# Optimization experiments

Measured on AMD Instinct MI355X. Metric: run time of the kernel, lower is better.

The kernel has to match this reference:

```python
import jax, jax.numpy as jnp
import numpy as np

N, E = 50000, 800000
D, H, EDIM, DFF = 128, 8, 16, 512
C = D // H  # per-head channels
NEG_SLOPE_GAT = 0.2
NEG_SLOPE = 0.01
EPS_LN = 1e-6


def layer_norm(x, g, b):
    mu = x.mean(-1, keepdims=True)
    sd = x.std(-1, keepdims=True, ddof=1)  # torch std default (unbiased)
    return g * (x - mu) / (sd + EPS_LN) + b


def gat_conv(x, ei, ew, W, a_src, a_dst, We, a_e, bias):
    # PyG GATConv with edge_dim, concat=True, eval mode (no dropout)
    n = x.shape[0]
    xh = (x @ W).reshape(n, H, C)            # [N,H,C]
    s_src = (xh * a_src).sum(-1)             # [N,H]
    s_dst = (xh * a_dst).sum(-1)             # [N,H]
    eh = (ew @ We).reshape(-1, H, C)         # [E,H,C]
    s_e = (eh * a_e).sum(-1)                 # [E,H]
    src, dst = ei[0], ei[1]
    alpha = jax.nn.leaky_relu(s_src[src] + s_dst[dst] + s_e, NEG_SLOPE_GAT)  # [E,H]
    # segment softmax over destination nodes
    m = jax.ops.segment_max(alpha, dst, num_segments=n)
    alpha = jnp.exp(alpha - m[dst])
    z = jax.ops.segment_sum(alpha, dst, num_segments=n)
    alpha = alpha / (z[dst] + 1e-16)
    msg = xh[src] * alpha[..., None]         # [E,H,C]
    out = jax.ops.segment_sum(msg, dst, num_segments=n)  # [N,H,C]
    return out.reshape(n, H * C) + bias


def setup_inputs() -> dict:
    key = jax.random.key(0)
    ks = jax.random.split(key, 32)
    p = lambda k, sh: (jax.random.normal(k, sh, dtype=jnp.float32) * 0.02)
    inp = {
        "nf": jax.random.normal(ks[0], (N, D), dtype=jnp.float32),
        "ei": jax.random.randint(ks[1], (2, E), 0, N, dtype=jnp.int32),
        "ew": jax.random.normal(ks[2], (E, EDIM), dtype=jnp.float32),
        # GATConv 1
        "W1": p(ks[3], (D, H * C)), "as1": p(ks[4], (H, C)), "ad1": p(ks[5], (H, C)),
        "We1": p(ks[6], (EDIM, H * C)), "ae1": p(ks[7], (H, C)), "b1": jnp.zeros((H * C,), jnp.float32),
        "g1": jnp.ones((D,), jnp.float32), "be1": jnp.zeros((D,), jnp.float32),
        # GATConv 2
        "W2": p(ks[8], (D, H * C)), "as2": p(ks[9], (H, C)), "ad2": p(ks[10], (H, C)),
        "We2": p(ks[11], (EDIM, H * C)), "ae2": p(ks[12], (H, C)), "b2": jnp.zeros((H * C,), jnp.float32),
        "g2": jnp.ones((D,), jnp.float32), "be2": jnp.zeros((D,), jnp.float32),
        # FFN + norm3
        "Wf1": p(ks[13], (D, DFF)), "bf1": jnp.zeros((DFF,), jnp.float32),
        "Wf2": p(ks[14], (DFF, D)), "bf2": jnp.zeros((D,), jnp.float32),
        "g3": jnp.ones((D,), jnp.float32), "be3": jnp.zeros((D,), jnp.float32),
    }
    return inp


def reference(nf, ei, ew, W1, as1, ad1, We1, ae1, b1, g1, be1,
              W2, as2, ad2, We2, ae2, b2, g2, be2,
              Wf1, bf1, Wf2, bf2, g3, be3):
    # gnn_mode == 'res', eval mode (dropout = identity)
    h = gat_conv(nf, ei, ew, W1, as1, ad1, We1, ae1, b1)
    nf = nf + jax.nn.leaky_relu(layer_norm(h, g1, be1), NEG_SLOPE)
    h = gat_conv(nf, ei, ew, W2, as2, ad2, We2, ae2, b2)
    nf = nf + jax.nn.leaky_relu(layer_norm(h, g2, be2), NEG_SLOPE)
    ff = jax.nn.relu(nf @ Wf1 + bf1) @ Wf2 + bf2
    nf = nf + jax.nn.leaky_relu(layer_norm(ff, g3, be3), NEG_SLOPE)
    return nf
```

## Files before the change

kernel.cpp:

```cpp
#include <hip/hip_runtime.h>
#include <hip/hip_bf16.h>

#define NN 50000
#define NE 800000
#define DD 128
#define HH 8
#define CC 16
#define DFF 512
#define ED 16
#define SCAN_NB ((NN + 255) / 256)
#define BKT 256
#define NBKT ((NN + BKT - 1) / BKT)
#define EPB 4096

typedef __attribute__((ext_vector_type(8))) short bf16x8;
typedef __attribute__((ext_vector_type(4))) float f32x4;

union U8 { bf16x8 v; unsigned short s[8]; };

__device__ inline unsigned short f2bf(float f) {
    union { float f; unsigned u; } v; v.f = f;
    return (unsigned short)((v.u + 0x7fffu + ((v.u >> 16) & 1u)) >> 16);
}
__device__ inline float bf2f(unsigned s) {
    union { unsigned u; float f; } v; v.u = s << 16;
    return v.f;
}

__global__ void zero_int_k(int* __restrict__ a, int n) {
    int i = blockIdx.x * 256 + threadIdx.x;
    if (i < n) a[i] = 0;
}

__global__ void cvtpack_k(const float* __restrict__ W, unsigned short* __restrict__ Wpk,
                          int K, int N) {
    int idx = blockIdx.x * 256 + threadIdx.x;
    if (idx >= K * N) return;
    int e = idx & 7;
    int l = (idx >> 3) & 63;
    int r = idx >> 9;
    int n16 = N >> 4;
    int jc = r % n16;
    int kt = r / n16;
    int k = kt * 32 + (l >> 4) * 8 + e;
    int n = jc * 16 + (l & 15);
    Wpk[idx] = f2bf(W[(size_t)k * N + n]);
}

__global__ void count_k(const int* __restrict__ dst, int* __restrict__ cnt) {
    int e = blockIdx.x * 256 + threadIdx.x;
    if (e < NE) atomicAdd(&cnt[dst[e]], 1);
}

__global__ void blksum_k(const int* __restrict__ cnt, int* __restrict__ partials) {
    int i = blockIdx.x * 256 + threadIdx.x;
    int v = (i < NN) ? cnt[i] : 0;
#pragma unroll
    for (int m = 1; m < 64; m <<= 1) v += __shfl_xor(v, m, 64);
    __shared__ int ws[4];
    if ((threadIdx.x & 63) == 0) ws[threadIdx.x >> 6] = v;
    __syncthreads();
    if (threadIdx.x == 0) partials[blockIdx.x] = ws[0] + ws[1] + ws[2] + ws[3];
}

__global__ void scanpart_k(int* __restrict__ partials) {
    __shared__ int buf[256];
    int t = threadIdx.x;
    int v = (t < SCAN_NB) ? partials[t] : 0;
    buf[t] = v;
    __syncthreads();
    for (int off = 1; off < 256; off <<= 1) {
        int u = (t >= off) ? buf[t - off] : 0;
        __syncthreads();
        buf[t] += u;
        __syncthreads();
    }
    if (t < SCAN_NB) partials[t] = buf[t] - v;
}

__global__ void scanapply_k(const int* __restrict__ cnt, const int* __restrict__ partials,
                            int* __restrict__ row_start, int* __restrict__ cursor) {
    __shared__ int buf[256];
    int t = threadIdx.x;
    int i = blockIdx.x * 256 + t;
    int v = (i < NN) ? cnt[i] : 0;
    buf[t] = v;
    __syncthreads();
    for (int off = 1; off < 256; off <<= 1) {
        int u = (t >= off) ? buf[t - off] : 0;
        __syncthreads();
        buf[t] += u;
        __syncthreads();
    }
    int excl = buf[t] - v + partials[blockIdx.x];
    if (i < NN) {
        row_start[i] = excl;
        cursor[i] = excl;
        if (i == NN - 1) row_start[NN] = excl + v;
    }
}

__global__ void bucketbase_k(const int* __restrict__ row_start, int* __restrict__ bucket_cursor) {
    int b = blockIdx.x * 256 + threadIdx.x;
    if (b < NBKT) bucket_cursor[b] = row_start[b * BKT];
}

__global__ __launch_bounds__(256) void bin_k(const int* __restrict__ ei,
                                             int* __restrict__ bucket_cursor,
                                             int2* __restrict__ binned) {
    __shared__ int hist[NBKT];
    __shared__ int base[NBKT];
    int t = threadIdx.x;
    int e0 = blockIdx.x * EPB;
    int eend = e0 + EPB; if (eend > NE) eend = NE;
    if (t < NBKT) hist[t] = 0;
    __syncthreads();
    for (int e = e0 + t; e < eend; e += 256) {
        int d = ei[NE + e];
        atomicAdd(&hist[d >> 8], 1);
    }
    __syncthreads();
    if (t < NBKT) {
        int c = hist[t];
        base[t] = c ? atomicAdd(&bucket_cursor[t], c) : 0;
        hist[t] = 0;
    }
    __syncthreads();
    for (int e = e0 + t; e < eend; e += 256) {
        int s = ei[e];
        int d = ei[NE + e];
        int b = d >> 8;
        int loc = atomicAdd(&hist[b], 1);
        binned[base[b] + loc] = make_int2(s | ((d & 255) << 16), e);
    }
}

__global__ __launch_bounds__(256) void csr_scatter_k(const int2* __restrict__ binned,
                                                     const int* __restrict__ row_start,
                                                     int* __restrict__ cursor,
                                                     int* __restrict__ e_src,
                                                     int* __restrict__ e_eid) {
    int b = blockIdx.x;
    int beg = row_start[b * BKT];
    int endNode = (b + 1) * BKT; if (endNode > NN) endNode = NN;
    int end = row_start[endNode];
    for (int p = beg + threadIdx.x; p < end; p += 256) {
        int2 r = binned[p];
        int d = b * BKT + (r.x >> 16);
        int pos = atomicAdd(&cursor[d], 1);
        e_src[pos] = r.x & 0xffff;
        e_eid[pos] = r.y;
    }
}

__global__ void se2_k(const float* __restrict__ ew, const int* __restrict__ e_eid,
                      const float* __restrict__ We1, const float* __restrict__ ae1,
                      const float* __restrict__ We2, const float* __restrict__ ae2,
                      unsigned short* __restrict__ s_e1, unsigned short* __restrict__ s_e2) {
    __shared__ float A1[ED * HH], A2[ED * HH];
    int t = threadIdx.x;
    if (t < 128) {
        int k = t >> 3, h = t & 7;
        float s = 0.f;
#pragma unroll
        for (int c = 0; c < CC; c++) s += We1[k * DD + h * CC + c] * ae1[h * CC + c];
        A1[t] = s;
    } else {
        int u = t - 128;
        int k = u >> 3, h = u & 7;
        float s = 0.f;
#pragma unroll
        for (int c = 0; c < CC; c++) s += We2[k * DD + h * CC + c] * ae2[h * CC + c];
        A2[u] = s;
    }
    __syncthreads();
    int p = blockIdx.x * 256 + t;
    if (p >= NE) return;
    int eid = e_eid[p];
    const float* ep = &ew[(size_t)eid * ED];
    float4 v0 = *(const float4*)(ep);
    float4 v1 = *(const float4*)(ep + 4);
    float4 v2 = *(const float4*)(ep + 8);
    float4 v3 = *(const float4*)(ep + 12);
    float ev[16] = {v0.x, v0.y, v0.z, v0.w, v1.x, v1.y, v1.z, v1.w,
                    v2.x, v2.y, v2.z, v2.w, v3.x, v3.y, v3.z, v3.w};
    float o1[8] = {0, 0, 0, 0, 0, 0, 0, 0};
    float o2[8] = {0, 0, 0, 0, 0, 0, 0, 0};
#pragma unroll
    for (int k = 0; k < 16; k++) {
        float v = ev[k];
#pragma unroll
        for (int h = 0; h < 8; h++) {
            o1[h] += v * A1[k * 8 + h];
            o2[h] += v * A2[k * 8 + h];
        }
    }
    U8 w1, w2;
#pragma unroll
    for (int h = 0; h < 8; h++) { w1.s[h] = f2bf(o1[h]); w2.s[h] = f2bf(o2[h]); }
    *(bf16x8*)&s_e1[(size_t)p * 8] = w1.v;
    *(bf16x8*)&s_e2[(size_t)p * 8] = w2.v;
}

__global__ __launch_bounds__(256) void gemm_mfma_k(const float* __restrict__ X,
                                                   const unsigned short* __restrict__ Wpk,
                                                   unsigned short* __restrict__ Ybf) {
    __shared__ char Xl[128 * 256];
    int t = threadIdx.x;
    int nb0 = blockIdx.x * 128;
    for (int c = t; c < 2048; c += 256) {
        int row = c >> 4, cb = c & 15;
        int n = nb0 + row;
        U8 u;
        if (n < NN) {
            const float* xp = &X[(size_t)n * DD + cb * 8];
            float4 a = *(const float4*)xp;
            float4 b = *(const float4*)(xp + 4);
            u.s[0] = f2bf(a.x); u.s[1] = f2bf(a.y); u.s[2] = f2bf(a.z); u.s[3] = f2bf(a.w);
            u.s[4] = f2bf(b.x); u.s[5] = f2bf(b.y); u.s[6] = f2bf(b.z); u.s[7] = f2bf(b.w);
        } else {
#pragma unroll
            for (int q = 0; q < 8; q++) u.s[q] = 0;
        }
        int byte = (row * 256 + cb * 16) ^ ((row & 7) << 4);
        *(bf16x8*)&Xl[byte] = u.v;
    }
    __syncthreads();
    int w = t >> 6, l = t & 63;
    int lrow = l & 15, lq = l >> 4;
    int r0 = (w & 1) * 64, c0 = (w >> 1) * 64;
    f32x4 acc[4][4];
#pragma unroll
    for (int i = 0; i < 4; i++)
#pragma unroll
        for (int j = 0; j < 4; j++) acc[i][j] = (f32x4){0.f, 0.f, 0.f, 0.f};
#pragma unroll
    for (int ks = 0; ks < 4; ks++) {
        int k0 = ks * 32;
        bf16x8 af[4], bq[4];
#pragma unroll
        for (int i = 0; i < 4; i++) {
            int rr = r0 + i * 16 + lrow;
            int byte = (rr * 256 + k0 * 2 + lq * 16) ^ ((rr & 7) << 4);
            af[i] = *(const bf16x8*)&Xl[byte];
        }
#pragma unroll
        for (int j = 0; j < 4; j++) {
            int j16 = (c0 >> 4) + j;
            bq[j] = *(const bf16x8*)&Wpk[(((size_t)ks * 8 + j16) * 64 + l) * 8];
        }
#pragma unroll
        for (int i = 0; i < 4; i++)
#pragma unroll
            for (int j = 0; j < 4; j++)
                acc[i][j] = __builtin_amdgcn_mfma_f32_16x16x32_bf16(af[i], bq[j], acc[i][j], 0, 0, 0);
    }
#pragma unroll
    for (int i = 0; i < 4; i++) {
#pragma unroll
        for (int j = 0; j < 4; j++) {
#pragma unroll
            for (int q = 0; q < 4; q++) {
                int n = nb0 + r0 + i * 16 + lq * 4 + q;
                if (n < NN) Ybf[(size_t)n * DD + c0 + j * 16 + lrow] = f2bf(acc[i][j][q]);
            }
        }
    }
}

__global__ void ssd_k(const unsigned short* __restrict__ xh_bf, const float* __restrict__ a_src,
                      const float* __restrict__ a_dst, unsigned short* __restrict__ s_srcb,
                      float* __restrict__ s_dst) {
    __shared__ float as[128], ad[128];
    if (threadIdx.x < 128) {
        as[threadIdx.x] = a_src[threadIdx.x];
        ad[threadIdx.x] = a_dst[threadIdx.x];
    }
    __syncthreads();
    int idx = blockIdx.x * 256 + threadIdx.x;
    if (idx >= NN * HH) return;
    int n = idx >> 3, h = idx & 7;
    const unsigned short* x = &xh_bf[(size_t)n * DD + h * CC];
    U8 u0, u1;
    u0.v = *(const bf16x8*)(x);
    u1.v = *(const bf16x8*)(x + 8);
    float s1 = 0.f, s2 = 0.f;
#pragma unroll
    for (int c = 0; c < 8; c++) {
        float v = bf2f(u0.s[c]);
        s1 += v * as[h * CC + c];
        s2 += v * ad[h * CC + c];
    }
#pragma unroll
    for (int c = 0; c < 8; c++) {
        float v = bf2f(u1.s[c]);
        s1 += v * as[h * CC + 8 + c];
        s2 += v * ad[h * CC + 8 + c];
    }
    s_srcb[idx] = f2bf(s1);
    s_dst[idx] = s2;
}

__global__ __launch_bounds__(256) void agg_ln_k(const int* __restrict__ row_start,
                                                const int* __restrict__ e_src,
                                                const unsigned short* __restrict__ s_srcb,
                                                const float* __restrict__ s_dst,
                                                const unsigned short* __restrict__ s_eb,
                                                const unsigned short* __restrict__ xh_bf,
                                                const float* __restrict__ bias,
                                                const float* __restrict__ g,
                                                const float* __restrict__ be,
                                                const float* __restrict__ res,
                                                float* __restrict__ outNf) {
    int wid = (blockIdx.x * 256 + threadIdx.x) >> 6;
    if (wid >= NN) return;
    int lane = threadIdx.x & 63;
    int h = lane >> 3;
    int k = lane & 7;
    unsigned h2 = (unsigned)h << 1;
    unsigned loff = (unsigned)lane << 2;
    const char* xb = (const char*)xh_bf;
    const char* sb = (const char*)s_srcb;
    const char* eb = (const char*)s_eb;
    float sdst = s_dst[wid * 8 + h];
    int beg = row_start[wid], end = row_start[wid + 1];
    float acc0 = 0.f, acc1 = 0.f, zpart = 0.f, ztail = 0.f;
    int p = beg;
    int bcast = h << 3;
    for (; p + 8 <= end; p += 8) {
        unsigned q = (unsigned)e_src[p + k];
        float vs = bf2f(*(const unsigned short*)(sb + (q << 4) + h2));
        float ve = bf2f(*(const unsigned short*)(eb + (((unsigned)(p + k)) << 4) + h2));
        float a = vs + sdst + ve;
        a = fmaxf(a, 0.2f * a);
        float esc = __expf(a);
        zpart += esc;
#pragma unroll
        for (int kk = 0; kk < 8; kk++) {
            float sck = __shfl(esc, bcast + kk, 64);
            unsigned qk = (unsigned)__shfl((int)q, kk, 64);
            unsigned u = *(const unsigned*)(xb + (qk << 8) + loff);
            acc0 = fmaf(sck, bf2f(u & 0xffffu), acc0);
            acc1 = fmaf(sck, bf2f(u >> 16), acc1);
        }
    }
    for (; p < end; p++) {
        unsigned q0 = (unsigned)e_src[p];
        float a0 = bf2f(*(const unsigned short*)(sb + (q0 << 4) + h2)) + sdst
                 + bf2f(*(const unsigned short*)(eb + ((unsigned)p << 4) + h2));
        unsigned u0 = *(const unsigned*)(xb + (q0 << 8) + loff);
        a0 = fmaxf(a0, 0.2f * a0);
        float e0 = __expf(a0);
        ztail += e0;
        acc0 = fmaf(e0, bf2f(u0 & 0xffffu), acc0);
        acc1 = fmaf(e0, bf2f(u0 >> 16), acc1);
    }
    float z = zpart;
    z += __shfl_xor(z, 1, 64);
    z += __shfl_xor(z, 2, 64);
    z += __shfl_xor(z, 4, 64);
    z += ztail;
    float inv = 1.f / (z + 1e-16f);
    float2 b = *(const float2*)&bias[lane * 2];
    float x0 = acc0 * inv + b.x;
    float x1 = acc1 * inv + b.y;
    float s = x0 + x1;
    float q = x0 * x0 + x1 * x1;
#pragma unroll
    for (int m = 1; m < 64; m <<= 1) {
        s += __shfl_xor(s, m, 64);
        q += __shfl_xor(q, m, 64);
    }
    float mu = s * (1.f / 128.f);
    float var = (q - 128.f * mu * mu) * (1.f / 127.f);
    float sd = sqrtf(fmaxf(var, 0.f));
    float invs = 1.f / (sd + 1e-6f);
    float2 gg = *(const float2*)&g[lane * 2];
    float2 bb = *(const float2*)&be[lane * 2];
    float y0 = gg.x * (x0 - mu) * invs + bb.x;
    float y1 = gg.y * (x1 - mu) * invs + bb.y;
    y0 = (y0 > 0.f) ? y0 : 0.01f * y0;
    y1 = (y1 > 0.f) ? y1 : 0.01f * y1;
    float2 r = *(const float2*)&res[(size_t)wid * DD + lane * 2];
    *(float2*)&outNf[(size_t)wid * DD + lane * 2] = make_float2(r.x + y0, r.y + y1);
}

__global__ __launch_bounds__(256) void ffn_ln_k(const float* __restrict__ X,
                                                const unsigned short* __restrict__ Wf1pk,
                                                const float* __restrict__ bf1,
                                                const unsigned short* __restrict__ Wf2pk,
                                                const float* __restrict__ bf2,
                                                const float* __restrict__ g3,
                                                const float* __restrict__ be3,
                                                float* __restrict__ out) {
    __shared__ char LDSBUF[32768];
    char* Xl = LDSBUF;
    char* Hl = LDSBUF + 16384;
    int t = threadIdx.x;
    int nb0 = blockIdx.x * 64;
    for (int c = t; c < 1024; c += 256) {
        int row = c >> 4, cb = c & 15;
        int n = nb0 + row;
        U8 u;
        if (n < NN) {
            const float* xp = &X[(size_t)n * DD + cb * 8];
            float4 a = *(const float4*)xp;
            float4 b = *(const float4*)(xp + 4);
            u.s[0] = f2bf(a.x); u.s[1] = f2bf(a.y); u.s[2] = f2bf(a.z); u.s[3] = f2bf(a.w);
            u.s[4] = f2bf(b.x); u.s[5] = f2bf(b.y); u.s[6] = f2bf(b.z); u.s[7] = f2bf(b.w);
        } else {
#pragma unroll
            for (int q = 0; q < 8; q++) u.s[q] = 0;
        }
        int byte = (row * 256 + cb * 16) ^ ((row & 7) << 4);
        *(bf16x8*)&Xl[byte] = u.v;
    }
    __syncthreads();
    int w = t >> 6, l = t & 63;
    int lrow = l & 15, lq = l >> 4;
    int wr = (w & 1) * 32;
    int wc = (w >> 1) * 64;
    f32x4 oacc[2][4];
#pragma unroll
    for (int i = 0; i < 2; i++)
#pragma unroll
        for (int j = 0; j < 4; j++) oacc[i][j] = (f32x4){0.f, 0.f, 0.f, 0.f};

#pragma unroll
    for (int ch = 0; ch < 4; ch++) {
        int hc0 = ch * 128;
        f32x4 a[2][4];
#pragma unroll
        for (int i = 0; i < 2; i++)
#pragma unroll
            for (int j = 0; j < 4; j++) a[i][j] = (f32x4){0.f, 0.f, 0.f, 0.f};
#pragma unroll
        for (int ks = 0; ks < 4; ks++) {
            int k0 = ks * 32;
            bf16x8 af[2], bq[4];
#pragma unroll
            for (int i = 0; i < 2; i++) {
                int rr = wr + i * 16 + lrow;
                int byte = (rr * 256 + k0 * 2 + lq * 16) ^ ((rr & 7) << 4);
                af[i] = *(const bf16x8*)&Xl[byte];
            }
#pragma unroll
            for (int j = 0; j < 4; j++) {
                int j16 = ch * 8 + (wc >> 4) + j;
                bq[j] = *(const bf16x8*)&Wf1pk[(((size_t)ks * 32 + j16) * 64 + l) * 8];
            }
#pragma unroll
            for (int i = 0; i < 2; i++)
#pragma unroll
                for (int j = 0; j < 4; j++)
                    a[i][j] = __builtin_amdgcn_mfma_f32_16x16x32_bf16(af[i], bq[j], a[i][j], 0, 0, 0);
        }
        float bias[4];
#pragma unroll
        for (int j = 0; j < 4; j++) bias[j] = bf1[hc0 + wc + j * 16 + lrow];
#pragma unroll
        for (int i = 0; i < 2; i++) {
#pragma unroll
            for (int j = 0; j < 4; j++) {
#pragma unroll
                for (int q = 0; q < 4; q++) {
                    float v = fmaxf(a[i][j][q] + bias[j], 0.f);
                    int row = wr + i * 16 + lq * 4 + q;
                    int col = wc + j * 16 + lrow;
                    int byte = (row * 256 + col * 2) ^ ((row & 7) << 4);
                    *(unsigned short*)&Hl[byte] = f2bf(v);
                }
            }
        }
        __syncthreads();
#pragma unroll
        for (int ks = 0; ks < 4; ks++) {
            int k0 = ks * 32;
            bf16x8 hf[2], b2[4];
#pragma unroll
            for (int i = 0; i < 2; i++) {
                int rr = wr + i * 16 + lrow;
                int byte = (rr * 256 + k0 * 2 + lq * 16) ^ ((rr & 7) << 4);
                hf[i] = *(const bf16x8*)&Hl[byte];
            }
#pragma unroll
            for (int j = 0; j < 4; j++) {
                int kt = ch * 4 + ks;
                int j16 = (wc >> 4) + j;
                b2[j] = *(const bf16x8*)&Wf2pk[(((size_t)kt * 8 + j16) * 64 + l) * 8];
            }
#pragma unroll
            for (int i = 0; i < 2; i++)
#pragma unroll
                for (int j = 0; j < 4; j++)
                    oacc[i][j] = __builtin_amdgcn_mfma_f32_16x16x32_bf16(hf[i], b2[j], oacc[i][j], 0, 0, 0);
        }
        __syncthreads();
    }
    float* Ol = (float*)LDSBUF;
#pragma unroll
    for (int i = 0; i < 2; i++) {
#pragma unroll
        for (int j = 0; j < 4; j++) {
#pragma unroll
            for (int q = 0; q < 4; q++) {
                int row = wr + i * 16 + lq * 4 + q;
                int col = wc + j * 16 + lrow;
                Ol[row * 128 + col] = oacc[i][j][q];
            }
        }
    }
    __syncthreads();
    float2 b = *(const float2*)&bf2[l * 2];
    float2 gg = *(const float2*)&g3[l * 2];
    float2 bb = *(const float2*)&be3[l * 2];
    for (int rr = w * 16; rr < w * 16 + 16; rr++) {
        int n = nb0 + rr;
        if (n >= NN) continue;
        float x0 = Ol[rr * 128 + l * 2]     + b.x;
        float x1 = Ol[rr * 128 + l * 2 + 1] + b.y;
        float s = x0 + x1;
        float q = x0 * x0 + x1 * x1;
#pragma unroll
        for (int m = 1; m < 64; m <<= 1) {
            s += __shfl_xor(s, m, 64);
            q += __shfl_xor(q, m, 64);
        }
        float mu = s * (1.f / 128.f);
        float var = (q - 128.f * mu * mu) * (1.f / 127.f);
        float sd = sqrtf(fmaxf(var, 0.f));
        float inv = 1.f / (sd + 1e-6f);
        float y0 = gg.x * (x0 - mu) * inv + bb.x;
        float y1 = gg.y * (x1 - mu) * inv + bb.y;
        y0 = (y0 > 0.f) ? y0 : 0.01f * y0;
        y1 = (y1 > 0.f) ? y1 : 0.01f * y1;
        float2 r = *(const float2*)&X[(size_t)n * DD + l * 2];
        *(float2*)&out[(size_t)n * DD + l * 2] = make_float2(r.x + y0, r.y + y1);
    }
}

extern "C" void kernel_launch(void* const* d_in, const int* in_sizes, int n_in,
                              void* d_out, int out_size, void* d_ws, size_t ws_size,
                              hipStream_t stream) {
    const float* nf  = (const float*)d_in[0];
    const int*   ei  = (const int*)d_in[1];
    const float* ew  = (const float*)d_in[2];
    const float* W1  = (const float*)d_in[3];
    const float* as1 = (const float*)d_in[4];
    const float* ad1 = (const float*)d_in[5];
    const float* We1 = (const float*)d_in[6];
    const float* ae1 = (const float*)d_in[7];
    const float* b1  = (const float*)d_in[8];
    const float* g1  = (const float*)d_in[9];
    const float* be1 = (const float*)d_in[10];
    const float* W2  = (const float*)d_in[11];
    const float* as2 = (const float*)d_in[12];
    const float* ad2 = (const float*)d_in[13];
    const float* We2 = (const float*)d_in[14];
    const float* ae2 = (const float*)d_in[15];
    const float* b2  = (const float*)d_in[16];
    const float* g2  = (const float*)d_in[17];
    const float* be2 = (const float*)d_in[18];
    const float* Wf1 = (const float*)d_in[19];
    const float* bf1 = (const float*)d_in[20];
    const float* Wf2 = (const float*)d_in[21];
    const float* bf2 = (const float*)d_in[22];
    const float* g3  = (const float*)d_in[23];
    const float* be3 = (const float*)d_in[24];
    float* out = (float*)d_out;

    char* p = (char*)d_ws;
    auto alloc = [&](size_t bytes) {
        char* r = p;
        p += (bytes + 255) & ~(size_t)255;
        return r;
    };
    float* nf_cur = (float*)alloc((size_t)NN * DD * 4);
    unsigned short* xh_bf = (unsigned short*)alloc((size_t)NN * DD * 2);
    unsigned short* s_e1  = (unsigned short*)alloc((size_t)NE * HH * 2);
    unsigned short* s_e2  = (unsigned short*)alloc((size_t)NE * HH * 2);
    unsigned short* s_srcb = (unsigned short*)alloc((size_t)NN * HH * 2);
    float* s_dst  = (float*)alloc((size_t)NN * HH * 4);
    int* row_start = (int*)alloc((size_t)(NN + 1) * 4);
    int* cnt       = (int*)alloc((size_t)NN * 4);
    int* cursor    = (int*)alloc((size_t)NN * 4);
    int* partials  = (int*)alloc((size_t)SCAN_NB * 4);
    int* bucket_cursor = (int*)alloc((size_t)NBKT * 4);
    int2* binned   = (int2*)alloc((size_t)NE * 8);
    int* e_src     = (int*)alloc((size_t)NE * 4);
    int* e_eid     = (int*)alloc((size_t)NE * 4);
    unsigned short* W1pk  = (unsigned short*)alloc((size_t)DD * DD * 2);
    unsigned short* W2pk  = (unsigned short*)alloc((size_t)DD * DD * 2);
    unsigned short* Wf1pk = (unsigned short*)alloc((size_t)DD * DFF * 2);
    unsigned short* Wf2pk = (unsigned short*)alloc((size_t)DFF * DD * 2);

    int ebl = (NE + 255) / 256;
    int nbl = (NN + 255) / 256;

    cvtpack_k<<<(DD * DD + 255) / 256, 256, 0, stream>>>(W1, W1pk, DD, DD);
    cvtpack_k<<<(DD * DD + 255) / 256, 256, 0, stream>>>(W2, W2pk, DD, DD);
    cvtpack_k<<<(DD * DFF + 255) / 256, 256, 0, stream>>>(Wf1, Wf1pk, DD, DFF);
    cvtpack_k<<<(DD * DFF + 255) / 256, 256, 0, stream>>>(Wf2, Wf2pk, DFF, DD);

    zero_int_k<<<nbl, 256, 0, stream>>>(cnt, NN);
    count_k<<<ebl, 256, 0, stream>>>(ei + NE, cnt);
    blksum_k<<<SCAN_NB, 256, 0, stream>>>(cnt, partials);
    scanpart_k<<<1, 256, 0, stream>>>(partials);
    scanapply_k<<<SCAN_NB, 256, 0, stream>>>(cnt, partials, row_start, cursor);

    bucketbase_k<<<(NBKT + 255) / 256, 256, 0, stream>>>(row_start, bucket_cursor);
    bin_k<<<(NE + EPB - 1) / EPB, 256, 0, stream>>>(ei, bucket_cursor, binned);
    csr_scatter_k<<<NBKT, 256, 0, stream>>>(binned, row_start, cursor, e_src, e_eid);

    se2_k<<<ebl, 256, 0, stream>>>(ew, e_eid, We1, ae1, We2, ae2, s_e1, s_e2);

    int gbl = (NN + 127) / 128;
    int wbl = (NN + 3) / 4;
    int sbl = (NN * HH + 255) / 256;

    gemm_mfma_k<<<gbl, 256, 0, stream>>>(nf, W1pk, xh_bf);
    ssd_k<<<sbl, 256, 0, stream>>>(xh_bf, as1, ad1, s_srcb, s_dst);
    agg_ln_k<<<wbl, 256, 0, stream>>>(row_start, e_src, s_srcb, s_dst, s_e1, xh_bf,
                                      b1, g1, be1, nf, nf_cur);

    gemm_mfma_k<<<gbl, 256, 0, stream>>>(nf_cur, W2pk, xh_bf);
    ssd_k<<<sbl, 256, 0, stream>>>(xh_bf, as2, ad2, s_srcb, s_dst);
    agg_ln_k<<<wbl, 256, 0, stream>>>(row_start, e_src, s_srcb, s_dst, s_e2, xh_bf,
                                      b2, g2, be2, nf_cur, nf_cur);

    ffn_ln_k<<<(NN + 63) / 64, 256, 0, stream>>>(nf_cur, Wf1pk, bf1, Wf2pk,
                                                 bf2, g3, be3, out);
}
```

Baseline: 295.4 us.

## Give each wave its own 16 rows in FFN kernel, removing block barriers

```diff
diff --git a/kernel.cpp b/kernel.cpp
--- a/kernel.cpp
+++ b/kernel.cpp
@@ -394,13 +394,17 @@
                                                 const float* __restrict__ be3,
                                                 float* __restrict__ out) {
     __shared__ char LDSBUF[32768];
-    char* Xl = LDSBUF;
-    char* Hl = LDSBUF + 16384;
     int t = threadIdx.x;
+    int w = t >> 6, l = t & 63;
+    int lrow = l & 15, lq = l >> 4;
     int nb0 = blockIdx.x * 64;
-    for (int c = t; c < 1024; c += 256) {
+    int rowbase = nb0 + w * 16;
+    char* Xw = LDSBUF + w * 4096;
+    char* Hw = LDSBUF + 16384 + w * 4096;
+
+    for (int c = l; c < 256; c += 64) {
         int row = c >> 4, cb = c & 15;
-        int n = nb0 + row;
+        int n = rowbase + row;
         U8 u;
         if (n < NN) {
             const float* xp = &X[(size_t)n * DD + cb * 8];
@@ -413,129 +417,100 @@
             for (int q = 0; q < 8; q++) u.s[q] = 0;
         }
         int byte = (row * 256 + cb * 16) ^ ((row & 7) << 4);
-        *(bf16x8*)&Xl[byte] = u.v;
-    }
-    __syncthreads();
-    int w = t >> 6, l = t & 63;
-    int lrow = l & 15, lq = l >> 4;
-    int wr = (w & 1) * 32;
-    int wc = (w >> 1) * 64;
-    f32x4 oacc[2][4];
-#pragma unroll
-    for (int i = 0; i < 2; i++)
-#pragma unroll
-        for (int j = 0; j < 4; j++) oacc[i][j] = (f32x4){0.f, 0.f, 0.f, 0.f};
+        *(bf16x8*)&Xw[byte] = u.v;
+    }
+
+    f32x4 oacc[8];
+#pragma unroll
+    for (int j = 0; j < 8; j++) oacc[j] = (f32x4){0.f, 0.f, 0.f, 0.f};
 
 #pragma unroll
     for (int ch = 0; ch < 4; ch++) {
-        int hc0 = ch * 128;
-        f32x4 a[2][4];
-#pragma unroll
-        for (int i = 0; i < 2; i++)
-#pragma unroll
-            for (int j = 0; j < 4; j++) a[i][j] = (f32x4){0.f, 0.f, 0.f, 0.f};
+        f32x4 a[8];
+#pragma unroll
+        for (int j = 0; j < 8; j++) a[j] = (f32x4){0.f, 0.f, 0.f, 0.f};
 #pragma unroll
         for (int ks = 0; ks < 4; ks++) {
-            int k0 = ks * 32;
-            bf16x8 af[2], bq[4];
-#pragma unroll
-            for (int i = 0; i < 2; i++) {
-                int rr = wr + i * 16 + lrow;
-                int byte = (rr * 256 + k0 * 2 + lq * 16) ^ ((rr & 7) << 4);
-                af[i] = *(const bf16x8*)&Xl[byte];
+            int byte = (lrow * 256 + ks * 64 + lq * 16) ^ ((lrow & 7) << 4);
+            bf16x8 af = *(const bf16x8*)&Xw[byte];
+#pragma unroll
+            for (int j = 0; j < 8; j++) {
+                int jc = ch * 8 + j;
+                bf16x8 bq = *(const bf16x8*)&Wf1pk[(((size_t)ks * 32 + jc) * 64 + l) * 8];
+                a[j] = __builtin_amdgcn_mfma_f32_16x16x32_bf16(af, bq, a[j], 0, 0, 0);
             }
-#pragma unroll
-            for (int j = 0; j < 4; j++) {
-                int j16 = ch * 8 + (wc >> 4) + j;
-                bq[j] = *(const bf16x8*)&Wf1pk[(((size_t)ks * 32 + j16) * 64 + l) * 8];
+        }
+#pragma unroll
+        for (int j = 0; j < 8; j++) {
+            float bias = bf1[ch * 128 + j * 16 + lrow];
+#pragma unroll
+            for (int q = 0; q < 4; q++) {
+                float v = fmaxf(a[j][q] + bias, 0.f);
+                int row = lq * 4 + q;
+                int col = j * 16 + lrow;
+                int byte = (row * 256 + col * 2) ^ ((row & 7) << 4);
+                *(unsigned short*)&Hw[byte] = f2bf(v);
             }
-#pragma unroll
-            for (int i = 0; i < 2; i++)
-#pragma unroll
-                for (int j = 0; j < 4; j++)
-                    a[i][j] = __builtin_amdgcn_mfma_f32_16x16x32_bf16(af[i], bq[j], a[i][j], 0, 0, 0);
-        }
-        float bias[4];
-#pragma unroll
-        for (int j = 0; j < 4; j++) bias[j] = bf1[hc0 + wc + j * 16 + lrow];
-#pragma unroll
-        for (int i = 0; i < 2; i++) {
-#pragma unroll
-            for (int j = 0; j < 4; j++) {
-#pragma unroll
-                for (int q = 0; q < 4; q++) {
-                    float v = fmaxf(a[i][j][q] + bias[j], 0.f);
-                    int row = wr + i * 16 + lq * 4 + q;
-                    int col = wc + j * 16 + lrow;
-                    int byte = (row * 256 + col * 2) ^ ((row & 7) << 4);
-                    *(unsigned short*)&Hl[byte] = f2bf(v);
-                }
+        }
+#pragma unroll
+        for (int ks = 0; ks < 4; ks++) {
+            int byte = (lrow * 256 + ks * 64 + lq * 16) ^ ((lrow & 7) << 4);
+            bf16x8 hf = *(const bf16x8*)&Hw[byte];
+            int kt = ch * 4 + ks;
+#pragma unroll
+            for (int j = 0; j < 8; j++) {
+                bf16x8 b2 = *(const bf16x8*)&Wf2pk[(((size_t)kt * 8 + j) * 64 + l) * 8];
+                oacc[j] = __builtin_amdgcn_mfma_f32_16x16x32_bf16(hf, b2, oacc[j], 0, 0, 0);
             }
         }
-        __syncthreads();
-#pragma unroll
-        for (int ks = 0; ks < 4; ks++) {
-            int k0 = ks * 32;
-            bf16x8 hf[2], b2[4];
-#pragma unroll
-            for (int i = 0; i < 2; i++) {
-                int rr = wr + i * 16 + lrow;
-                int byte = (rr * 256 + k0 * 2 + lq * 16) ^ ((rr & 7) << 4);
-                hf[i] = *(const bf16x8*)&Hl[byte];
-            }
-#pragma unroll
-            for (int j = 0; j < 4; j++) {
-                int kt = ch * 4 + ks;
-                int j16 = (wc >> 4) + j;
-                b2[j] = *(const bf16x8*)&Wf2pk[(((size_t)kt * 8 + j16) * 64 + l) * 8];
-            }
-#pragma unroll
-            for (int i = 0; i < 2; i++)
-#pragma unroll
-                for (int j = 0; j < 4; j++)
-                    oacc[i][j] = __builtin_amdgcn_mfma_f32_16x16x32_bf16(hf[i], b2[j], oacc[i][j], 0, 0, 0);
-        }
-        __syncthreads();
-    }
-    float* Ol = (float*)LDSBUF;
-#pragma unroll
-    for (int i = 0; i < 2; i++) {
-#pragma unroll
-        for (int j = 0; j < 4; j++) {
-#pragma unroll
-            for (int q = 0; q < 4; q++) {
-                int row = wr + i * 16 + lq * 4 + q;
-                int col = wc + j * 16 + lrow;
-                Ol[row * 128 + col] = oacc[i][j][q];
-            }
-        }
-    }
-    __syncthreads();
-    float2 b = *(const float2*)&bf2[l * 2];
-    float2 gg = *(const float2*)&g3[l * 2];
-    float2 bb = *(const float2*)&be3[l * 2];
-    for (int rr = w * 16; rr < w * 16 + 16; rr++) {
-        int n = nb0 + rr;
+    }
+
+    float bcol[8], gcol[8], becol[8];
+#pragma unroll
+    for (int j = 0; j < 8; j++) {
+        int col = j * 16 + lrow;
+        bcol[j] = bf2[col];
+        gcol[j] = g3[col];
+        becol[j] = be3[col];
+    }
+    float sum[4], sq[4];
+#pragma unroll
+    for (int q = 0; q < 4; q++) {
+        float s = 0.f, qq = 0.f;
+#pragma unroll
+        for (int j = 0; j < 8; j++) {
+            float x = oacc[j][q] + bcol[j];
+            s += x;
+            qq += x * x;
+        }
+        sum[q] = s;
+        sq[q] = qq;
+    }
+#pragma unroll
+    for (int m = 1; m < 16; m <<= 1) {
+#pragma unroll
+        for (int q = 0; q < 4; q++) {
+            sum[q] += __shfl_xor(sum[q], m, 64);
+            sq[q]  += __shfl_xor(sq[q], m, 64);
+        }
+    }
+#pragma unroll
+    for (int q = 0; q < 4; q++) {
+        int n = rowbase + lq * 4 + q;
         if (n >= NN) continue;
-        float x0 = Ol[rr * 128 + l * 2]     + b.x;
-        float x1 = Ol[rr * 128 + l * 2 + 1] + b.y;
-        float s = x0 + x1;
-        float q = x0 * x0 + x1 * x1;
-#pragma unroll
-        for (int m = 1; m < 64; m <<= 1) {
-            s += __shfl_xor(s, m, 64);
-            q += __shfl_xor(q, m, 64);
-        }
-        float mu = s * (1.f / 128.f);
-        float var = (q - 128.f * mu * mu) * (1.f / 127.f);
+        float mu = sum[q] * (1.f / 128.f);
+        float var = (sq[q] - 128.f * mu * mu) * (1.f / 127.f);
         float sd = sqrtf(fmaxf(var, 0.f));
         float inv = 1.f / (sd + 1e-6f);
-        float y0 = gg.x * (x0 - mu) * inv + bb.x;
-        float y1 = gg.y * (x1 - mu) * inv + bb.y;
-        y0 = (y0 > 0.f) ? y0 : 0.01f * y0;
-        y1 = (y1 > 0.f) ? y1 : 0.01f * y1;
-        float2 r = *(const float2*)&X[(size_t)n * DD + l * 2];
-        *(float2*)&out[(size_t)n * DD + l * 2] = make_float2(r.x + y0, r.y + y1);
+#pragma unroll
+        for (int j = 0; j < 8; j++) {
+            int col = j * 16 + lrow;
+            float x = oacc[j][q] + bcol[j];
+            float y = gcol[j] * (x - mu) * inv + becol[j];
+            y = (y > 0.f) ? y : 0.01f * y;
+            float r = X[(size_t)n * DD + col];
+            out[(size_t)n * DD + col] = r + y;
+        }
     }
 }
 
```

After: 285.9 us. 3.2% less time.
